# Optimization experiments

Measured on AMD Instinct MI355X. Metric: run time of the kernel, lower is better.

## Reference

```python
import jax, jax.numpy as jnp
import numpy as np

B, S, D, H = 2, 2048, 1024, 16
DK = D // H


def setup_inputs() -> dict:
    key = jax.random.key(0)
    ks = jax.random.split(key, 12)
    s = 1.0 / np.sqrt(D)
    return {
        "query": jax.random.normal(ks[0], (B, S, D), dtype=jnp.float32),
        "key": jax.random.normal(ks[1], (B, S, D), dtype=jnp.float32),
        "value": jax.random.normal(ks[2], (B, S, D), dtype=jnp.float32),
        "mask": jax.random.randint(ks[3], (B, 1, 1, S), 0, 2, dtype=jnp.int32),
        "wq": jax.random.normal(ks[4], (D, D), dtype=jnp.float32) * s,
        "bq": jnp.zeros((D,), dtype=jnp.float32),
        "wk": jax.random.normal(ks[5], (D, D), dtype=jnp.float32) * s,
        "bk": jnp.zeros((D,), dtype=jnp.float32),
        "wv": jax.random.normal(ks[6], (D, D), dtype=jnp.float32) * s,
        "bv": jnp.zeros((D,), dtype=jnp.float32),
        "wo": jax.random.normal(ks[7], (D, D), dtype=jnp.float32) * s,
        "bo": jnp.zeros((D,), dtype=jnp.float32),
    }


def reference(query, key, value, mask, wq, bq, wk, bk, wv, bv, wo, bo):
    b, s, d = query.shape
    # torch Linear: y = x @ W^T + b, then split heads -> [B, H, S, dk]
    def proj(x, w, bias):
        return (x @ w.T + bias).reshape(b, -1, H, DK).transpose(0, 2, 1, 3)

    q = proj(query, wq, bq)
    k = proj(key, wk, bk)
    v = proj(value, wv, bv)

    scores = jnp.einsum("bhqd,bhkd->bhqk", q, k) / jnp.sqrt(jnp.float32(DK))
    scores = jnp.where(mask == 0, jnp.float32(-1e9), scores)
    attn = jax.nn.softmax(scores, axis=-1)  # [B,H,S,S]
    x = jnp.einsum("bhqk,bhkd->bhqd", attn, v)
    x = x.transpose(0, 2, 1, 3).reshape(b, s, d)
    return x @ wo.T + bo
```

## Files before the change

kernel.cpp:

```cpp
#include <hip/hip_runtime.h>
#include <math.h>

#define B_  2
#define S_  2048
#define D_  1024
#define H_  16
#define DK_ 64
#define NT_ (S_ / 64)

typedef unsigned short u16;
typedef unsigned int u32;
typedef __bf16 bf16x8 __attribute__((ext_vector_type(8)));
typedef float f32x4 __attribute__((ext_vector_type(4)));

typedef const __attribute__((address_space(1))) void* gas1_t;
typedef __attribute__((address_space(3))) void* las3_t;

__device__ __forceinline__ void gload_lds16(const void* g, void* l) {
    __builtin_amdgcn_global_load_lds((gas1_t)g, (las3_t)l, 16, 0, 0);
}

__device__ __forceinline__ u16 f2bf(float f) {
    union { float f; unsigned u; } v; v.f = f;
    return (u16)((v.u + 0x7fffu + ((v.u >> 16) & 1u)) >> 16);
}

__device__ __forceinline__ u32 pack_bf16_2(float lo, float hi) {
    union { float f; u32 u; } a, b;
    a.f = lo; b.f = hi;
    return __builtin_amdgcn_perm(b.u + 0x8000u, a.u + 0x8000u, 0x07060302u);
}

__global__ __launch_bounds__(256)
void cast_all(const float* __restrict__ q, const float* __restrict__ k,
              const float* __restrict__ v, const float* __restrict__ wq,
              const float* __restrict__ wk, const float* __restrict__ wv,
              const float* __restrict__ wo, const int* __restrict__ mask,
              u16* __restrict__ qb, u16* __restrict__ kb, u16* __restrict__ vb,
              u16* __restrict__ wqb, u16* __restrict__ wkb, u16* __restrict__ wvb,
              u16* __restrict__ wob, float* __restrict__ mbias)
{
    const int i = blockIdx.x * 256 + threadIdx.x;
    if (i >= 4194304) {
        const int idx = i - 4194304;
        mbias[idx] = mask[idx] ? 0.0f : -1e9f;
        return;
    }
    const float* src; u16* dst; int off;
    if (i < 3 * 1048576) {
        const int seg = i >> 20; off = i & 1048575;
        src = (seg == 0) ? q : (seg == 1) ? k : v;
        dst = (seg == 0) ? qb : (seg == 1) ? kb : vb;
    } else {
        const int j = i - 3 * 1048576;
        const int seg = j >> 18; off = j & 262143;
        src = (seg == 0) ? wq : (seg == 1) ? wk : (seg == 2) ? wv : wo;
        dst = (seg == 0) ? wqb : (seg == 1) ? wkb : (seg == 2) ? wvb : wob;
    }
    const float4 val = ((const float4*)src)[off];
    uint2 o;
    o.x = pack_bf16_2(val.x, val.y);
    o.y = pack_bf16_2(val.z, val.w);
    ((uint2*)dst)[off] = o;
}

template<int BN>
__device__ __forceinline__ void gemm_body(
    const u16* __restrict__ A, const u16* __restrict__ W,
    const float* __restrict__ bias, void* __restrict__ outp,
    float scale, int mode, int m0, int n0)
{
    constexpr int NJ = BN / 32;
    __shared__ u16 sA[128 * 32];
    __shared__ u16 sW[BN * 32];

    const int tid  = threadIdx.x;
    const int wave = tid >> 6, lane = tid & 63;
    const int quad = lane >> 4, l16 = lane & 15;
    const int wm = (wave >> 1) * 64;
    const int wn = (wave & 1) * (BN / 2);
    const int lrow = lane >> 2;
    const int lcol = (lane & 3) * 8;

    f32x4 acc[4][NJ];
    const f32x4 zero = {0.f, 0.f, 0.f, 0.f};
#pragma unroll
    for (int i = 0; i < 4; ++i)
#pragma unroll
        for (int j = 0; j < NJ; ++j) acc[i][j] = zero;

    for (int k0 = 0; k0 < D_; k0 += 32) {
        const int t0 = wave, t1 = wave + 4;
        gload_lds16(A + (size_t)(m0 + t0 * 16 + lrow) * D_ + k0 + lcol, sA + t0 * 512);
        gload_lds16(A + (size_t)(m0 + t1 * 16 + lrow) * D_ + k0 + lcol, sA + t1 * 512);
        if (BN == 128) {
            gload_lds16(W + (size_t)(n0 + t0 * 16 + lrow) * D_ + k0 + lcol, sW + t0 * 512);
            gload_lds16(W + (size_t)(n0 + t1 * 16 + lrow) * D_ + k0 + lcol, sW + t1 * 512);
        } else {
            gload_lds16(W + (size_t)(n0 + wave * 16 + lrow) * D_ + k0 + lcol, sW + wave * 512);
        }
        __syncthreads();

        bf16x8 af[4], bfr[NJ];
#pragma unroll
        for (int i = 0; i < 4; ++i)
            af[i] = *(const bf16x8*)(sA + (wm + i * 16 + l16) * 32 + quad * 8);
#pragma unroll
        for (int j = 0; j < NJ; ++j)
            bfr[j] = *(const bf16x8*)(sW + (wn + j * 16 + l16) * 32 + quad * 8);
#pragma unroll
        for (int i = 0; i < 4; ++i)
#pragma unroll
            for (int j = 0; j < NJ; ++j)
                acc[i][j] = __builtin_amdgcn_mfma_f32_16x16x32_bf16(af[i], bfr[j], acc[i][j], 0, 0, 0);
        __syncthreads();
    }

#pragma unroll
    for (int i = 0; i < 4; ++i) {
#pragma unroll
        for (int j = 0; j < NJ; ++j) {
            const int n = n0 + wn + j * 16 + l16;
            if (mode == 3) {
#pragma unroll
                for (int r = 0; r < 4; ++r) {
                    const int mp = m0 + wm + i * 16 + quad * 4 + r;
                    ((u16*)outp)[(size_t)mp * (B_ * S_) + n] = f2bf(acc[i][j][r] + bias[mp]);
                }
            } else {
                const float bn = bias[n];
#pragma unroll
                for (int r = 0; r < 4; ++r) {
                    const int m = m0 + wm + i * 16 + quad * 4 + r;
                    const float v = acc[i][j][r] + bn;
                    if (mode == 0) {
                        ((float*)outp)[(size_t)m * D_ + n] = v;
                    } else {
                        const int b = m >> 11, s = m & (S_ - 1);
                        const int h = n >> 6, dk = n & 63;
                        ((u16*)outp)[(((size_t)(b * H_ + h)) * S_ + s) * DK_ + dk] = f2bf(v * scale);
                    }
                }
            }
        }
    }
}

__global__ __launch_bounds__(256)
void qkv_gemm(const u16* __restrict__ qin, const u16* __restrict__ kin, const u16* __restrict__ vin,
              const u16* __restrict__ wqb, const u16* __restrict__ wkb, const u16* __restrict__ wvb,
              const float* __restrict__ bq, const float* __restrict__ bk, const float* __restrict__ bv,
              u16* __restrict__ Qp, u16* __restrict__ Kp, u16* __restrict__ Vt)
{
    const int z = blockIdx.z;
    if (z == 2) {
        gemm_body<128>(wvb, vin, bv, Vt, 1.0f, 3, blockIdx.x * 128, blockIdx.y * 128);
    } else {
        const u16* A = (z == 0) ? qin : kin;
        const u16* W = (z == 0) ? wqb : wkb;
        const float* bias = (z == 0) ? bq : bk;
        u16* outp = (z == 0) ? Qp : Kp;
        const float scale = (z == 0) ? 0.18033688011112042f : 1.0f;
        gemm_body<128>(A, W, bias, outp, scale, 1, blockIdx.y * 128, blockIdx.x * 128);
    }
}

__global__ __launch_bounds__(256)
void out_gemm(const u16* __restrict__ Xc, const u16* __restrict__ wob,
              const float* __restrict__ bo, float* __restrict__ out)
{
    gemm_body<64>(Xc, wob, bo, out, 1.0f, 0, blockIdx.y * 128, blockIdx.x * 64);
}

__global__ __launch_bounds__(256)
void attn_mfma(const u16* __restrict__ Qp, const u16* __restrict__ Kp,
               const u16* __restrict__ Vt, const float* __restrict__ mbias,
               u16* __restrict__ Xc)
{
    __shared__ u16 sQ[128 * 64];
    __shared__ u16 sK[2][64 * 64];
    __shared__ u16 sV[2][64 * 64];

    const int tid  = threadIdx.x;
    const int wave = tid >> 6, lane = tid & 63;
    const int quad = lane >> 4, l16 = lane & 15;
    const int qt = blockIdx.x & 15;
    const int bh = blockIdx.x >> 4;
    const int b  = bh >> 4;
    const int h  = bh & 15;
    const int srow = lane >> 3;
    const int scol = ((lane & 7) ^ srow) * 8;
    const int sw7  = l16 & 7;

    const u16* Qb = Qp + ((size_t)bh * S_ + qt * 128) * DK_;
    const u16* Kb = Kp + (size_t)bh * S_ * DK_;
    const u16* Vb = Vt + ((size_t)h * 64) * (B_ * S_) + b * S_;
    const float* mbf = mbias + b * S_;

#pragma unroll
    for (int t = 0; t < 4; ++t) {
        const int tt = wave + t * 4;
        gload_lds16(Qb + (size_t)(tt * 8 + srow) * DK_ + scol, sQ + tt * 512);
    }
#pragma unroll
    for (int t = 0; t < 2; ++t) {
        const int tt = wave + t * 4;
        gload_lds16(Kb + (size_t)(tt * 8 + srow) * DK_ + scol, &sK[0][tt * 512]);
        gload_lds16(Vb + (size_t)(tt * 8 + srow) * (B_ * S_) + scol, &sV[0][tt * 512]);
    }
    __syncthreads();

    bf16x8 qf[2][2];
#pragma unroll
    for (int iq = 0; iq < 2; ++iq)
#pragma unroll
        for (int ks = 0; ks < 2; ++ks) {
            const int row = wave * 32 + iq * 16 + l16;
            const int phys = (ks * 4 + quad) ^ sw7;
            qf[iq][ks] = *(const bf16x8*)(sQ + row * 64 + phys * 8);
        }
    u16* sPw = sQ + wave * 2048;

    f32x4 oacc[2][4];
    const f32x4 zero = {0.f, 0.f, 0.f, 0.f};
#pragma unroll
    for (int im = 0; im < 2; ++im)
#pragma unroll
        for (int nd = 0; nd < 4; ++nd) oacc[im][nd] = zero;
    f32x4 lsum4[2] = {zero, zero};

    float4 mk4[4];
#pragma unroll
    for (int in = 0; in < 4; ++in)
        mk4[in] = *(const float4*)(mbf + in * 16 + quad * 4);

    for (int kt = 0; kt < NT_; ++kt) {
        __syncthreads();
        const int cur = kt & 1;

        if (kt < NT_ - 1) {
            const int alt = cur ^ 1;
#pragma unroll
            for (int t = 0; t < 2; ++t) {
                const int tt = wave + t * 4;
                gload_lds16(Kb + (size_t)((kt + 1) * 64 + tt * 8 + srow) * DK_ + scol, &sK[alt][tt * 512]);
                gload_lds16(Vb + (size_t)(tt * 8 + srow) * (B_ * S_) + (kt + 1) * 64 + scol, &sV[alt][tt * 512]);
            }
        }
        float4 mkn[4];
        const int ktn = (kt < NT_ - 1) ? kt + 1 : kt;
#pragma unroll
        for (int in = 0; in < 4; ++in)
            mkn[in] = *(const float4*)(mbf + ktn * 64 + in * 16 + quad * 4);

        f32x4 sfr[2][4];
#pragma unroll
        for (int iq = 0; iq < 2; ++iq)
#pragma unroll
            for (int in = 0; in < 4; ++in) {
                sfr[iq][in][0] = mk4[in].x;
                sfr[iq][in][1] = mk4[in].y;
                sfr[iq][in][2] = mk4[in].z;
                sfr[iq][in][3] = mk4[in].w;
            }

#pragma unroll
        for (int in = 0; in < 4; ++in) {
#pragma unroll
            for (int ks = 0; ks < 2; ++ks) {
                const int phys = (ks * 4 + quad) ^ sw7;
                const bf16x8 kf = *(const bf16x8*)(&sK[cur][(in * 16 + l16) * 64 + phys * 8]);
#pragma unroll
                for (int iq = 0; iq < 2; ++iq)
                    sfr[iq][in] = __builtin_amdgcn_mfma_f32_16x16x32_bf16(kf, qf[iq][ks], sfr[iq][in], 0, 0, 0);
            }
        }

#pragma unroll
        for (int iq = 0; iq < 2; ++iq) {
#pragma unroll
            for (int in = 0; in < 4; ++in) {
                const float p0 = __builtin_amdgcn_exp2f(sfr[iq][in][0]);
                const float p1 = __builtin_amdgcn_exp2f(sfr[iq][in][1]);
                const float p2 = __builtin_amdgcn_exp2f(sfr[iq][in][2]);
                const float p3 = __builtin_amdgcn_exp2f(sfr[iq][in][3]);
                lsum4[iq][in] += (p0 + p1) + (p2 + p3);
                uint2 o;
                o.x = pack_bf16_2(p0, p1);
                o.y = pack_bf16_2(p2, p3);
                const int pchunk = (in * 2 + (quad >> 1)) ^ sw7;
                *(uint2*)(sPw + (iq * 16 + l16) * 64 + pchunk * 8 + (quad & 1) * 4) = o;
            }
        }
#pragma unroll
        for (int in = 0; in < 4; ++in) mk4[in] = mkn[in];

#pragma unroll
        for (int ks = 0; ks < 2; ++ks) {
            bf16x8 pf[2];
#pragma unroll
            for (int im = 0; im < 2; ++im) {
                const int phys = (ks * 4 + quad) ^ sw7;
                pf[im] = *(const bf16x8*)(sPw + (im * 16 + l16) * 64 + phys * 8);
            }
#pragma unroll
            for (int nd = 0; nd < 4; ++nd) {
                const int phys = (ks * 4 + quad) ^ sw7;
                const bf16x8 vf = *(const bf16x8*)(&sV[cur][(nd * 16 + l16) * 64 + phys * 8]);
#pragma unroll
                for (int im = 0; im < 2; ++im)
                    oacc[im][nd] = __builtin_amdgcn_mfma_f32_16x16x32_bf16(pf[im], vf, oacc[im][nd], 0, 0, 0);
            }
        }
    }

    float lq[2];
#pragma unroll
    for (int iq = 0; iq < 2; ++iq) {
        float v = (lsum4[iq][0] + lsum4[iq][1]) + (lsum4[iq][2] + lsum4[iq][3]);
        v += __shfl_xor(v, 16);
        v += __shfl_xor(v, 32);
        lq[iq] = v;
    }
    float* sL = (float*)sPw;
    if (quad == 0) {
        sL[l16] = lq[0];
        sL[16 + l16] = lq[1];
    }
    float linv[2][4];
#pragma unroll
    for (int im = 0; im < 2; ++im)
#pragma unroll
        for (int r = 0; r < 4; ++r)
            linv[im][r] = __builtin_amdgcn_rcpf(sL[im * 16 + quad * 4 + r]);

#pragma unroll
    for (int im = 0; im < 2; ++im)
#pragma unroll
        for (int r = 0; r < 4; ++r) {
            const int s = qt * 128 + wave * 32 + im * 16 + quad * 4 + r;
            const float inv = linv[im][r];
#pragma unroll
            for (int nd = 0; nd < 4; ++nd)
                Xc[((size_t)(b * S_ + s)) * D_ + h * 64 + nd * 16 + l16] =
                    f2bf(oacc[im][nd][r] * inv);
        }
}

extern "C" void kernel_launch(void* const* d_in, const int* in_sizes, int n_in,
                              void* d_out, int out_size, void* d_ws, size_t ws_size,
                              hipStream_t stream)
{
    (void)in_sizes; (void)n_in; (void)out_size; (void)ws_size;

    const float* query = (const float*)d_in[0];
    const float* key   = (const float*)d_in[1];
    const float* value = (const float*)d_in[2];
    const int*   mask  = (const int*)d_in[3];
    const float* wq    = (const float*)d_in[4];
    const float* bq    = (const float*)d_in[5];
    const float* wk    = (const float*)d_in[6];
    const float* bk    = (const float*)d_in[7];
    const float* wv    = (const float*)d_in[8];
    const float* bv    = (const float*)d_in[9];
    const float* wo    = (const float*)d_in[10];
    const float* bo    = (const float*)d_in[11];

    const size_t NE = (size_t)B_ * S_ * D_;
    const size_t WE = (size_t)D_ * D_;

    u16* qb  = (u16*)d_ws;
    u16* kb  = qb + NE;
    u16* vb  = kb + NE;
    u16* wqb = vb + NE;
    u16* wkb = wqb + WE;
    u16* wvb = wkb + WE;
    u16* wob = wvb + WE;
    u16* Qp  = wob + WE;
    u16* Kp  = Qp + NE;
    u16* Vt  = Kp + NE;
    float* mbias = (float*)(Vt + NE);
    u16* Xc  = qb;

    cast_all<<<16400, 256, 0, stream>>>(query, key, value, wq, wk, wv, wo, mask,
                                        qb, kb, vb, wqb, wkb, wvb, wob, mbias);

    qkv_gemm<<<dim3(D_ / 128, (B_ * S_) / 128, 3), 256, 0, stream>>>(
        qb, kb, vb, wqb, wkb, wvb, bq, bk, bv, Qp, Kp, Vt);

    attn_mfma<<<dim3(B_ * H_ * (S_ / 128)), 256, 0, stream>>>(Qp, Kp, Vt, mbias, Xc);

    out_gemm<<<dim3(D_ / 64, (B_ * S_) / 128), 256, 0, stream>>>(Xc, wob, bo, (float*)d_out);
}
```

Measured before the change: 242.2 us.

## Fold attention mask into K/V projections and compute row sums with MFMA

Masked keys are handled upstream instead of inside the attention loop. The K projection rows and V projection columns for masked positions are zeroed, so those keys score 0 and contribute exp(0)=1 to the denominator but nothing to the output. The per-batch count of masked keys is then subtracted from the row sum. Row sums are now taken with an extra MFMA against a ones vector on the bf16 P tile, which removes the per-tile mask-bias loads, the VALU sum accumulation and the shuffle reduction. Separately, the projection GEMMs move to a 64-wide K step with an XOR-swizzled LDS layout. The trade-offs: the denominator is summed from bf16-rounded probabilities with a subtraction that can cancel, and a fully masked row would divide by zero.

```diff
diff --git a/kernel.cpp b/kernel.cpp
--- a/kernel.cpp
+++ b/kernel.cpp
@@ -38,14 +38,33 @@
               const float* __restrict__ wo, const int* __restrict__ mask,
               u16* __restrict__ qb, u16* __restrict__ kb, u16* __restrict__ vb,
               u16* __restrict__ wqb, u16* __restrict__ wkb, u16* __restrict__ wvb,
-              u16* __restrict__ wob, float* __restrict__ mbias)
-{
-    const int i = blockIdx.x * 256 + threadIdx.x;
-    if (i >= 4194304) {
-        const int idx = i - 4194304;
-        mbias[idx] = mask[idx] ? 0.0f : -1e9f;
+              u16* __restrict__ wob, float* __restrict__ mfac,
+              float* __restrict__ nmaskf)
+{
+    const int bi = blockIdx.x;
+    const int tid = threadIdx.x;
+    if (bi >= 16400) {
+        const int b = bi - 16400;
+        __shared__ int red[256];
+        int c = 0;
+#pragma unroll
+        for (int j = 0; j < 8; ++j)
+            c += (mask[b * S_ + tid * 8 + j] == 0) ? 1 : 0;
+        red[tid] = c;
+        __syncthreads();
+        for (int s = 128; s > 0; s >>= 1) {
+            if (tid < s) red[tid] += red[tid + s];
+            __syncthreads();
+        }
+        if (tid == 0) nmaskf[b] = (float)red[0];
         return;
     }
+    if (bi >= 16384) {
+        const int idx = (bi - 16384) * 256 + tid;
+        mfac[idx] = mask[idx] ? 1.0f : 0.0f;
+        return;
+    }
+    const int i = bi * 256 + tid;
     const float* src; u16* dst; int off;
     if (i < 3 * 1048576) {
         const int seg = i >> 20; off = i & 1048575;
@@ -68,19 +87,21 @@
 __device__ __forceinline__ void gemm_body(
     const u16* __restrict__ A, const u16* __restrict__ W,
     const float* __restrict__ bias, void* __restrict__ outp,
-    float scale, int mode, int m0, int n0)
+    float scale, int mode, int m0, int n0,
+    const float* __restrict__ rowfac, const float* __restrict__ colfac)
 {
     constexpr int NJ = BN / 32;
-    __shared__ u16 sA[128 * 32];
-    __shared__ u16 sW[BN * 32];
+    __shared__ u16 sA[128 * 64];
+    __shared__ u16 sW[BN * 64];
 
     const int tid  = threadIdx.x;
     const int wave = tid >> 6, lane = tid & 63;
     const int quad = lane >> 4, l16 = lane & 15;
     const int wm = (wave >> 1) * 64;
     const int wn = (wave & 1) * (BN / 2);
-    const int lrow = lane >> 2;
-    const int lcol = (lane & 3) * 8;
+    const int srow = lane >> 3;
+    const int scol = ((lane & 7) ^ srow) * 8;
+    const int sw7  = l16 & 7;
 
     f32x4 acc[4][NJ];
     const f32x4 zero = {0.f, 0.f, 0.f, 0.f};
@@ -89,56 +110,75 @@
 #pragma unroll
         for (int j = 0; j < NJ; ++j) acc[i][j] = zero;
 
-    for (int k0 = 0; k0 < D_; k0 += 32) {
-        const int t0 = wave, t1 = wave + 4;
-        gload_lds16(A + (size_t)(m0 + t0 * 16 + lrow) * D_ + k0 + lcol, sA + t0 * 512);
-        gload_lds16(A + (size_t)(m0 + t1 * 16 + lrow) * D_ + k0 + lcol, sA + t1 * 512);
+    const u16* ast = A + (size_t)(m0 + wave * 8 + srow) * D_ + scol;
+    const u16* wst = W + (size_t)(n0 + wave * 8 + srow) * D_ + scol;
+
+    for (int k0 = 0; k0 < D_; k0 += 64) {
+#pragma unroll
+        for (int t = 0; t < 4; ++t)
+            gload_lds16(ast + (size_t)t * 32 * D_ + k0, sA + (wave + t * 4) * 512);
         if (BN == 128) {
-            gload_lds16(W + (size_t)(n0 + t0 * 16 + lrow) * D_ + k0 + lcol, sW + t0 * 512);
-            gload_lds16(W + (size_t)(n0 + t1 * 16 + lrow) * D_ + k0 + lcol, sW + t1 * 512);
+#pragma unroll
+            for (int t = 0; t < 4; ++t)
+                gload_lds16(wst + (size_t)t * 32 * D_ + k0, sW + (wave + t * 4) * 512);
         } else {
-            gload_lds16(W + (size_t)(n0 + wave * 16 + lrow) * D_ + k0 + lcol, sW + wave * 512);
+#pragma unroll
+            for (int t = 0; t < 2; ++t)
+                gload_lds16(wst + (size_t)t * 32 * D_ + k0, sW + (wave + t * 4) * 512);
         }
         __syncthreads();
 
-        bf16x8 af[4], bfr[NJ];
-#pragma unroll
-        for (int i = 0; i < 4; ++i)
-            af[i] = *(const bf16x8*)(sA + (wm + i * 16 + l16) * 32 + quad * 8);
-#pragma unroll
-        for (int j = 0; j < NJ; ++j)
-            bfr[j] = *(const bf16x8*)(sW + (wn + j * 16 + l16) * 32 + quad * 8);
-#pragma unroll
-        for (int i = 0; i < 4; ++i)
+#pragma unroll
+        for (int kh = 0; kh < 2; ++kh) {
+            const int phys = ((kh * 4 + quad) ^ sw7) * 8;
+            bf16x8 af[4], bfr[NJ];
+#pragma unroll
+            for (int i = 0; i < 4; ++i)
+                af[i] = *(const bf16x8*)(sA + (wm + i * 16 + l16) * 64 + phys);
 #pragma unroll
             for (int j = 0; j < NJ; ++j)
-                acc[i][j] = __builtin_amdgcn_mfma_f32_16x16x32_bf16(af[i], bfr[j], acc[i][j], 0, 0, 0);
+                bfr[j] = *(const bf16x8*)(sW + (wn + j * 16 + l16) * 64 + phys);
+#pragma unroll
+            for (int i = 0; i < 4; ++i)
+#pragma unroll
+                for (int j = 0; j < NJ; ++j)
+                    acc[i][j] = __builtin_amdgcn_mfma_f32_16x16x32_bf16(af[i], bfr[j], acc[i][j], 0, 0, 0);
+        }
         __syncthreads();
     }
 
 #pragma unroll
     for (int i = 0; i < 4; ++i) {
+        float rf4[4];
+        if (mode == 1 && rowfac) {
+#pragma unroll
+            for (int r = 0; r < 4; ++r)
+                rf4[r] = rowfac[m0 + wm + i * 16 + quad * 4 + r];
+        }
 #pragma unroll
         for (int j = 0; j < NJ; ++j) {
             const int n = n0 + wn + j * 16 + l16;
             if (mode == 3) {
+                const float cf = colfac ? colfac[n] : 1.0f;
 #pragma unroll
                 for (int r = 0; r < 4; ++r) {
                     const int mp = m0 + wm + i * 16 + quad * 4 + r;
-                    ((u16*)outp)[(size_t)mp * (B_ * S_) + n] = f2bf(acc[i][j][r] + bias[mp]);
+                    ((u16*)outp)[(size_t)mp * (B_ * S_) + n] = f2bf((acc[i][j][r] + bias[mp]) * cf);
                 }
             } else {
                 const float bn = bias[n];
 #pragma unroll
                 for (int r = 0; r < 4; ++r) {
                     const int m = m0 + wm + i * 16 + quad * 4 + r;
-                    const float v = acc[i][j][r] + bn;
+                    float v = acc[i][j][r] + bn;
                     if (mode == 0) {
                         ((float*)outp)[(size_t)m * D_ + n] = v;
                     } else {
+                        v *= scale;
+                        if (rowfac) v *= rf4[r];
                         const int b = m >> 11, s = m & (S_ - 1);
                         const int h = n >> 6, dk = n & 63;
-                        ((u16*)outp)[(((size_t)(b * H_ + h)) * S_ + s) * DK_ + dk] = f2bf(v * scale);
+                        ((u16*)outp)[(((size_t)(b * H_ + h)) * S_ + s) * DK_ + dk] = f2bf(v);
                     }
                 }
             }
@@ -150,18 +190,22 @@
 void qkv_gemm(const u16* __restrict__ qin, const u16* __restrict__ kin, const u16* __restrict__ vin,
               const u16* __restrict__ wqb, const u16* __restrict__ wkb, const u16* __restrict__ wvb,
               const float* __restrict__ bq, const float* __restrict__ bk, const float* __restrict__ bv,
-              u16* __restrict__ Qp, u16* __restrict__ Kp, u16* __restrict__ Vt)
+              u16* __restrict__ Qp, u16* __restrict__ Kp, u16* __restrict__ Vt,
+              const float* __restrict__ mfac)
 {
     const int z = blockIdx.z;
     if (z == 2) {
-        gemm_body<128>(wvb, vin, bv, Vt, 1.0f, 3, blockIdx.x * 128, blockIdx.y * 128);
+        gemm_body<128>(wvb, vin, bv, Vt, 1.0f, 3, blockIdx.x * 128, blockIdx.y * 128,
+                       nullptr, mfac);
     } else {
         const u16* A = (z == 0) ? qin : kin;
         const u16* W = (z == 0) ? wqb : wkb;
         const float* bias = (z == 0) ? bq : bk;
         u16* outp = (z == 0) ? Qp : Kp;
         const float scale = (z == 0) ? 0.18033688011112042f : 1.0f;
-        gemm_body<128>(A, W, bias, outp, scale, 1, blockIdx.y * 128, blockIdx.x * 128);
+        const float* rf = (z == 1) ? mfac : nullptr;
+        gemm_body<128>(A, W, bias, outp, scale, 1, blockIdx.y * 128, blockIdx.x * 128,
+                       rf, nullptr);
     }
 }
 
@@ -169,12 +213,13 @@
 void out_gemm(const u16* __restrict__ Xc, const u16* __restrict__ wob,
               const float* __restrict__ bo, float* __restrict__ out)
 {
-    gemm_body<64>(Xc, wob, bo, out, 1.0f, 0, blockIdx.y * 128, blockIdx.x * 64);
+    gemm_body<64>(Xc, wob, bo, out, 1.0f, 0, blockIdx.y * 128, blockIdx.x * 64,
+                  nullptr, nullptr);
 }
 
 __global__ __launch_bounds__(256)
 void attn_mfma(const u16* __restrict__ Qp, const u16* __restrict__ Kp,
-               const u16* __restrict__ Vt, const float* __restrict__ mbias,
+               const u16* __restrict__ Vt, const float* __restrict__ nmaskf,
                u16* __restrict__ Xc)
 {
     __shared__ u16 sQ[128 * 64];
@@ -195,13 +240,11 @@
     const u16* Qb = Qp + ((size_t)bh * S_ + qt * 128) * DK_;
     const u16* Kb = Kp + (size_t)bh * S_ * DK_;
     const u16* Vb = Vt + ((size_t)h * 64) * (B_ * S_) + b * S_;
-    const float* mbf = mbias + b * S_;
-
-#pragma unroll
-    for (int t = 0; t < 4; ++t) {
-        const int tt = wave + t * 4;
-        gload_lds16(Qb + (size_t)(tt * 8 + srow) * DK_ + scol, sQ + tt * 512);
-    }
+
+#pragma unroll
+    for (int t = 0; t < 4; ++t)
+        gload_lds16(Qb + (size_t)((wave + t * 4) * 8 + srow) * DK_ + scol,
+                    sQ + (wave + t * 4) * 512);
 #pragma unroll
     for (int t = 0; t < 2; ++t) {
         const int tt = wave + t * 4;
@@ -221,58 +264,47 @@
         }
     u16* sPw = sQ + wave * 2048;
 
+    bf16x8 vones;
+#pragma unroll
+    for (int j = 0; j < 8; ++j) vones[j] = (__bf16)1.0f;
+
     f32x4 oacc[2][4];
     const f32x4 zero = {0.f, 0.f, 0.f, 0.f};
 #pragma unroll
     for (int im = 0; im < 2; ++im)
 #pragma unroll
         for (int nd = 0; nd < 4; ++nd) oacc[im][nd] = zero;
-    f32x4 lsum4[2] = {zero, zero};
-
-    float4 mk4[4];
-#pragma unroll
-    for (int in = 0; in < 4; ++in)
-        mk4[in] = *(const float4*)(mbf + in * 16 + quad * 4);
+    f32x4 lfrag[2] = {zero, zero};
+
+    const u16* kpre = Kb + (size_t)64 * DK_ + (size_t)(wave * 8 + srow) * DK_ + scol;
+    const u16* vpre = Vb + 64 + (size_t)(wave * 8 + srow) * (B_ * S_) + scol;
 
     for (int kt = 0; kt < NT_; ++kt) {
         __syncthreads();
         const int cur = kt & 1;
 
         if (kt < NT_ - 1) {
-            const int alt = cur ^ 1;
-#pragma unroll
-            for (int t = 0; t < 2; ++t) {
-                const int tt = wave + t * 4;
-                gload_lds16(Kb + (size_t)((kt + 1) * 64 + tt * 8 + srow) * DK_ + scol, &sK[alt][tt * 512]);
-                gload_lds16(Vb + (size_t)(tt * 8 + srow) * (B_ * S_) + (kt + 1) * 64 + scol, &sV[alt][tt * 512]);
-            }
-        }
-        float4 mkn[4];
-        const int ktn = (kt < NT_ - 1) ? kt + 1 : kt;
-#pragma unroll
-        for (int in = 0; in < 4; ++in)
-            mkn[in] = *(const float4*)(mbf + ktn * 64 + in * 16 + quad * 4);
+            u16* kdst = &sK[cur ^ 1][wave * 512];
+            u16* vdst = &sV[cur ^ 1][wave * 512];
+            gload_lds16(kpre, kdst);
+            gload_lds16(kpre + (size_t)32 * DK_, kdst + 4 * 512);
+            gload_lds16(vpre, vdst);
+            gload_lds16(vpre + (size_t)32 * (B_ * S_), vdst + 4 * 512);
+            kpre += (size_t)64 * DK_;
+            vpre += 64;
+        }
 
         f32x4 sfr[2][4];
 #pragma unroll
-        for (int iq = 0; iq < 2; ++iq)
-#pragma unroll
-            for (int in = 0; in < 4; ++in) {
-                sfr[iq][in][0] = mk4[in].x;
-                sfr[iq][in][1] = mk4[in].y;
-                sfr[iq][in][2] = mk4[in].z;
-                sfr[iq][in][3] = mk4[in].w;
-            }
-
-#pragma unroll
         for (int in = 0; in < 4; ++in) {
-#pragma unroll
-            for (int ks = 0; ks < 2; ++ks) {
-                const int phys = (ks * 4 + quad) ^ sw7;
-                const bf16x8 kf = *(const bf16x8*)(&sK[cur][(in * 16 + l16) * 64 + phys * 8]);
-#pragma unroll
-                for (int iq = 0; iq < 2; ++iq)
-                    sfr[iq][in] = __builtin_amdgcn_mfma_f32_16x16x32_bf16(kf, qf[iq][ks], sfr[iq][in], 0, 0, 0);
+            const int p0 = (quad ^ sw7) * 8;
+            const int p1 = ((4 + quad) ^ sw7) * 8;
+            const bf16x8 kf0 = *(const bf16x8*)(&sK[cur][(in * 16 + l16) * 64 + p0]);
+            const bf16x8 kf1 = *(const bf16x8*)(&sK[cur][(in * 16 + l16) * 64 + p1]);
+#pragma unroll
+            for (int iq = 0; iq < 2; ++iq) {
+                f32x4 t = __builtin_amdgcn_mfma_f32_16x16x32_bf16(kf0, qf[iq][0], zero, 0, 0, 0);
+                sfr[iq][in] = __builtin_amdgcn_mfma_f32_16x16x32_bf16(kf1, qf[iq][1], t, 0, 0, 0);
             }
         }
 
@@ -284,7 +316,6 @@
                 const float p1 = __builtin_amdgcn_exp2f(sfr[iq][in][1]);
                 const float p2 = __builtin_amdgcn_exp2f(sfr[iq][in][2]);
                 const float p3 = __builtin_amdgcn_exp2f(sfr[iq][in][3]);
-                lsum4[iq][in] += (p0 + p1) + (p2 + p3);
                 uint2 o;
                 o.x = pack_bf16_2(p0, p1);
                 o.y = pack_bf16_2(p2, p3);
@@ -292,21 +323,20 @@
                 *(uint2*)(sPw + (iq * 16 + l16) * 64 + pchunk * 8 + (quad & 1) * 4) = o;
             }
         }
-#pragma unroll
-        for (int in = 0; in < 4; ++in) mk4[in] = mkn[in];
 
 #pragma unroll
         for (int ks = 0; ks < 2; ++ks) {
+            const int phys = ((ks * 4 + quad) ^ sw7) * 8;
             bf16x8 pf[2];
 #pragma unroll
-            for (int im = 0; im < 2; ++im) {
-                const int phys = (ks * 4 + quad) ^ sw7;
-                pf[im] = *(const bf16x8*)(sPw + (im * 16 + l16) * 64 + phys * 8);
-            }
+            for (int im = 0; im < 2; ++im)
+                pf[im] = *(const bf16x8*)(sPw + (im * 16 + l16) * 64 + phys);
+#pragma unroll
+            for (int im = 0; im < 2; ++im)
+                lfrag[im] = __builtin_amdgcn_mfma_f32_16x16x32_bf16(pf[im], vones, lfrag[im], 0, 0, 0);
 #pragma unroll
             for (int nd = 0; nd < 4; ++nd) {
-                const int phys = (ks * 4 + quad) ^ sw7;
-                const bf16x8 vf = *(const bf16x8*)(&sV[cur][(nd * 16 + l16) * 64 + phys * 8]);
+                const bf16x8 vf = *(const bf16x8*)(&sV[cur][(nd * 16 + l16) * 64 + phys]);
 #pragma unroll
                 for (int im = 0; im < 2; ++im)
                     oacc[im][nd] = __builtin_amdgcn_mfma_f32_16x16x32_bf16(pf[im], vf, oacc[im][nd], 0, 0, 0);
@@ -314,25 +344,13 @@
         }
     }
 
-    float lq[2];
-#pragma unroll
-    for (int iq = 0; iq < 2; ++iq) {
-        float v = (lsum4[iq][0] + lsum4[iq][1]) + (lsum4[iq][2] + lsum4[iq][3]);
-        v += __shfl_xor(v, 16);
-        v += __shfl_xor(v, 32);
-        lq[iq] = v;
-    }
-    float* sL = (float*)sPw;
-    if (quad == 0) {
-        sL[l16] = lq[0];
-        sL[16 + l16] = lq[1];
-    }
+    const float nm = nmaskf[b];
     float linv[2][4];
 #pragma unroll
     for (int im = 0; im < 2; ++im)
 #pragma unroll
         for (int r = 0; r < 4; ++r)
-            linv[im][r] = __builtin_amdgcn_rcpf(sL[im * 16 + quad * 4 + r]);
+            linv[im][r] = __builtin_amdgcn_rcpf(lfrag[im][r] - nm);
 
 #pragma unroll
     for (int im = 0; im < 2; ++im)
@@ -379,16 +397,17 @@
     u16* Qp  = wob + WE;
     u16* Kp  = Qp + NE;
     u16* Vt  = Kp + NE;
-    float* mbias = (float*)(Vt + NE);
+    float* mfac   = (float*)(Vt + NE);
+    float* nmaskf = mfac + 4096;
     u16* Xc  = qb;
 
-    cast_all<<<16400, 256, 0, stream>>>(query, key, value, wq, wk, wv, wo, mask,
-                                        qb, kb, vb, wqb, wkb, wvb, wob, mbias);
+    cast_all<<<16402, 256, 0, stream>>>(query, key, value, wq, wk, wv, wo, mask,
+                                        qb, kb, vb, wqb, wkb, wvb, wob, mfac, nmaskf);
 
     qkv_gemm<<<dim3(D_ / 128, (B_ * S_) / 128, 3), 256, 0, stream>>>(
-        qb, kb, vb, wqb, wkb, wvb, bq, bk, bv, Qp, Kp, Vt);
-
-    attn_mfma<<<dim3(B_ * H_ * (S_ / 128)), 256, 0, stream>>>(Qp, Kp, Vt, mbias, Xc);
+        qb, kb, vb, wqb, wkb, wvb, bq, bk, bv, Qp, Kp, Vt, mfac);
+
+    attn_mfma<<<dim3(B_ * H_ * (S_ / 128)), 256, 0, stream>>>(Qp, Kp, Vt, nmaskf, Xc);
 
     out_gemm<<<dim3(D_ / 64, (B_ * S_) / 128), 256, 0, stream>>>(Xc, wob, bo, (float*)d_out);
 }
```

Result: no change. 240.4 us (-0.8%).
